# Kernel tuning notes

Hardware: AMD Instinct MI355X
Metric: run time of the kernel (lower is better)

## Reference

```python
import jax, jax.numpy as jnp
import numpy as np

N, E = 100000, 1600000
NODE_DIM, EDGE_DIM, HIDDEN = 64, 32, 64


def setup_inputs() -> dict:
    key = jax.random.key(0)
    ks = jax.random.split(key, 12)
    def lin(k, fan_in, fan_out):
        bound = 1.0 / np.sqrt(fan_in)
        kw, kb = jax.random.split(k)
        W = jax.random.uniform(kw, (fan_in, fan_out), jnp.float32, -bound, bound)
        b = jax.random.uniform(kb, (fan_out,), jnp.float32, -bound, bound)
        return W, b
    h = jax.random.normal(ks[0], (N, NODE_DIM), jnp.float32)
    edge_index = jax.random.randint(ks[1], (2, E), 0, N, jnp.int64 if jax.config.jax_enable_x64 else jnp.int32)
    edge_feat = jax.random.normal(ks[2], (E, EDGE_DIM), jnp.float32)
    eW1, eb1 = lin(ks[3], 2 * NODE_DIM + EDGE_DIM, HIDDEN)
    eW2, eb2 = lin(ks[4], HIDDEN, HIDDEN)
    uW1, ub1 = lin(ks[5], NODE_DIM + HIDDEN, HIDDEN)
    uW2, ub2 = lin(ks[6], HIDDEN, HIDDEN)
    return {"h": h, "edge_index": edge_index, "edge_feat": edge_feat,
            "eW1": eW1, "eb1": eb1, "eW2": eW2, "eb2": eb2,
            "uW1": uW1, "ub1": ub1, "uW2": uW2, "ub2": ub2}


def reference(h, edge_index, edge_feat, eW1, eb1, eW2, eb2, uW1, ub1, uW2, ub2):
    src, tgt = edge_index[0], edge_index[1]
    # gather endpoint features, concat with edge features: (E, 2*node_dim+edge_dim)
    inp = jnp.concatenate([h[src], h[tgt], edge_feat], axis=-1)
    # edge MLP: Linear -> ReLU -> Linear
    messages = jax.nn.relu(inp @ eW1 + eb1) @ eW2 + eb2  # (E, hidden)
    # scatter-add aggregation onto target nodes
    agg = jax.ops.segment_sum(messages, tgt, num_segments=h.shape[0])  # (N, hidden)
    # update MLP on [h || agg]
    upd_in = jnp.concatenate([h, agg], axis=-1)
    out = jax.nn.relu(upd_in @ uW1 + ub1) @ uW2 + ub2  # (N, hidden)
    return out
```

## Files before the change

### kernel.cpp

```cpp
#include <hip/hip_runtime.h>
#include <hip/hip_bf16.h>


typedef __attribute__((ext_vector_type(8))) short s16x8;
typedef __attribute__((ext_vector_type(4))) float f32x4;
typedef __attribute__((ext_vector_type(8))) unsigned short u16x8;

#define SXE 168
#define SXN 136
#define SX2 72
#define NBLK_EDGE 768
#define S1_CHUNK 4096
#define S2_CAP 10240

__device__ __forceinline__ unsigned short f2bf(float f) {
  __hip_bfloat16 b = __float2bfloat16(f);
  return __builtin_bit_cast(unsigned short, b);
}
__device__ __forceinline__ float bf2f(unsigned short s) {
  unsigned int u = ((unsigned int)s) << 16;
  return __builtin_bit_cast(float, u);
}
__device__ __forceinline__ u16x8 pack8(const float4 a, const float4 b) {
  u16x8 r;
  r[0] = f2bf(a.x); r[1] = f2bf(a.y); r[2] = f2bf(a.z); r[3] = f2bf(a.w);
  r[4] = f2bf(b.x); r[5] = f2bf(b.y); r[6] = f2bf(b.z); r[7] = f2bf(b.w);
  return r;
}

__device__ __forceinline__ void bar_lgkm() {
  __builtin_amdgcn_sched_barrier(0);
  asm volatile("s_waitcnt lgkmcnt(0)" ::: "memory");
  __builtin_amdgcn_s_barrier();
  __builtin_amdgcn_sched_barrier(0);
}

__global__ void prep(const float* __restrict__ h, unsigned short* __restrict__ hb, long long htot,
                     const float* __restrict__ eW1, const float* __restrict__ eW2,
                     const float* __restrict__ uW1, const float* __restrict__ uW2,
                     unsigned short* __restrict__ w1p, unsigned short* __restrict__ w2p,
                     unsigned short* __restrict__ uw1p, unsigned short* __restrict__ uw2p,
                     const int* __restrict__ ei, int* __restrict__ bhist, int E,
                     int conv_blocks) {
  __shared__ int lh[256];
  const int b = blockIdx.x;
  const int tid = threadIdx.x;
  if (b < conv_blocks) {
    const long long i = ((long long)b * 256 + tid) * 4;
    if (i + 3 < htot) {
      const float4 v = *(const float4*)(h + i);
      ushort4 o;
      o.x = f2bf(v.x); o.y = f2bf(v.y); o.z = f2bf(v.z); o.w = f2bf(v.w);
      *(ushort4*)(hb + i) = o;
    } else {
      for (long long j = i; j < htot; ++j) hb[j] = f2bf(h[j]);
    }
  } else if (b < conv_blocks + 13) {
    const int t2 = (b - conv_blocks) * 256 + tid;
    if (t2 < 52 * 64) {
      const int c = t2 & 63;
      int kg = t2 >> 6;
      const float* src;
      unsigned short* dst;
      if (kg < 20)      { src = eW1; dst = w1p; }
      else if (kg < 28) { src = eW2; dst = w2p; kg -= 20; }
      else if (kg < 44) { src = uW1; dst = uw1p; kg -= 28; }
      else              { src = uW2; dst = uw2p; kg -= 44; }
#pragma unroll
      for (int e = 0; e < 8; ++e)
        dst[(size_t)(kg * 64 + c) * 8 + e] = f2bf(src[(size_t)(kg * 8 + e) * 64 + c]);
    }
  } else {
    lh[tid] = 0;
    __syncthreads();
    const int hbk = b - conv_blocks - 13;
    for (long long e = (long long)hbk * 256 + tid; e < E; e += 1024LL * 256)
      atomicAdd(&lh[ei[E + e] >> 9], 1);
    __syncthreads();
    if (lh[tid]) atomicAdd(&bhist[tid], lh[tid]);
  }
}

__global__ void bscan(const int* __restrict__ bhist, int* __restrict__ bstart,
                      int* __restrict__ bcursor, int nbuck) {
  __shared__ int s[256];
  const int tid = threadIdx.x;
  const int v = (tid < nbuck) ? bhist[tid] : 0;
  s[tid] = v;
  __syncthreads();
  for (int off = 1; off < 256; off <<= 1) {
    int t = (tid >= off) ? s[tid - off] : 0;
    __syncthreads();
    s[tid] += t;
    __syncthreads();
  }
  const int excl = s[tid] - v;
  if (tid < nbuck) { bstart[tid] = excl; bcursor[tid] = excl; }
}

__global__ __launch_bounds__(256)
void bucket_scatter(const int* __restrict__ ei, int* __restrict__ bcursor,
                    unsigned long long* __restrict__ bufA, int E) {
  __shared__ int lhist[256], lbase[256], lcur[256];
  const int tid = threadIdx.x;
  const long long c0 = (long long)blockIdx.x * S1_CHUNK;

  lhist[tid] = 0;
  __syncthreads();

  unsigned long long rec[16];
  int bk[16];
#pragma unroll
  for (int j = 0; j < 16; ++j) {
    const long long e = c0 + j * 256 + tid;
    if (e < E) {
      const int t = ei[E + e];
      const int s = ei[e];
      rec[j] = (unsigned long long)(unsigned int)e |
               ((unsigned long long)(unsigned int)t << 21) |
               ((unsigned long long)(unsigned int)s << 38);
      bk[j] = t >> 9;
      atomicAdd(&lhist[bk[j]], 1);
    } else {
      bk[j] = -1;
    }
  }
  __syncthreads();

  if (lhist[tid] > 0) lbase[tid] = atomicAdd(&bcursor[tid], lhist[tid]);
  lcur[tid] = 0;
  __syncthreads();

#pragma unroll
  for (int j = 0; j < 16; ++j) {
    if (bk[j] >= 0) {
      const int pos = lbase[bk[j]] + atomicAdd(&lcur[bk[j]], 1);
      bufA[pos] = rec[j];
    }
  }
}

__global__ __launch_bounds__(256)
void bucket_sort(const unsigned long long* __restrict__ bufA,
                 const int* __restrict__ bstart, const int* __restrict__ bhist,
                 unsigned long long* __restrict__ aoe) {
  __shared__ unsigned long long srec[S2_CAP];
  __shared__ int khist[512];
  __shared__ int sdata[256];
  const int b = blockIdx.x;
  const int tid = threadIdx.x;
  const int s0 = bstart[b];
  const int nb = bhist[b];

  if (nb > S2_CAP) {
    for (int i = tid; i < nb; i += 256) aoe[s0 + i] = bufA[s0 + i];
    return;
  }

  khist[tid] = 0;
  khist[tid + 256] = 0;
  __syncthreads();
  for (int i = tid; i < nb; i += 256) {
    const unsigned long long r = bufA[s0 + i];
    atomicAdd(&khist[(int)((r >> 21) & 511)], 1);
  }
  __syncthreads();

  const int a0 = khist[2 * tid], a1 = khist[2 * tid + 1];
  const int sum = a0 + a1;
  sdata[tid] = sum;
  __syncthreads();
  for (int off = 1; off < 256; off <<= 1) {
    int t = (tid >= off) ? sdata[tid - off] : 0;
    __syncthreads();
    sdata[tid] += t;
    __syncthreads();
  }
  const int excl = sdata[tid] - sum;
  khist[2 * tid] = excl;
  khist[2 * tid + 1] = excl + a0;
  __syncthreads();

  for (int i = tid; i < nb; i += 256) {
    const unsigned long long r = bufA[s0 + i];
    const int pos = atomicAdd(&khist[(int)((r >> 21) & 511)], 1);
    srec[pos] = r;
  }
  __syncthreads();
  for (int i = tid; i < nb; i += 256) aoe[s0 + i] = srec[i];
}

__global__ __launch_bounds__(256, 4)
void edge_mlp_fused(const unsigned short* __restrict__ hb, const float* __restrict__ ef,
                    const unsigned short* __restrict__ w1p, const float* __restrict__ b1,
                    const unsigned short* __restrict__ w2p, const float* __restrict__ b2,
                    const unsigned long long* __restrict__ aoe, float* __restrict__ agg,
                    int E, int ntiles, int nblk) {
  __shared__ unsigned short X[64 * SXE];
  __shared__ unsigned short X2[64 * SX2];
  __shared__ unsigned short W2L[64 * 64];
  __shared__ int tgts[2][64];

  const int tid = threadIdx.x;
  const int w = tid >> 6, lane = tid & 63;
  const int g = lane >> 4, r = lane & 15;
  const int row = tid >> 2, q = tid & 3;

  {
    const int i = tid * 16;
    *(u16x8*)&W2L[i] = *(const u16x8*)&w2p[i];
    *(u16x8*)&W2L[i + 8] = *(const u16x8*)&w2p[i + 8];
  }

  const int t0 = (int)((long long)blockIdx.x * ntiles / nblk);
  const int t1 = (int)((long long)(blockIdx.x + 1) * ntiles / nblk);
  if (t0 >= t1) return;

  const long long Emax = (long long)E - 1;
  const int cb = w * 16;

  s16x8 bfrag1[5];
#pragma unroll
  for (int kk = 0; kk < 5; ++kk)
    bfrag1[kk] = *(const s16x8*)(w1p + (size_t)((kk * 4 + g) * 64 + cb + r) * 8);
  const float bias1 = b1[cb + r];
  float b2v[4];
#pragma unroll
  for (int nb = 0; nb < 4; ++nb) b2v[nb] = b2[nb * 16 + r];

  unsigned long long nxt_aoe;
  u16x8 hs0, hs1, ht0, ht1;
  float4 fea, feb;

  auto load_aoe = [&](int t) -> unsigned long long {
    long long p = (long long)t * 64 + row;
    if (p > Emax) p = Emax;
    return aoe[p];
  };
  auto issue_gathers = [&](const unsigned long long u) {
    const int s = (int)(u >> 38);
    const int t = (int)((u >> 21) & 0x1FFFF);
    const int e = (int)(u & 0x1FFFFF);
    const u16x8* hs = (const u16x8*)(hb + (size_t)s * 64);
    const u16x8* ht = (const u16x8*)(hb + (size_t)t * 64);
    hs0 = hs[2 * q]; hs1 = hs[2 * q + 1];
    ht0 = ht[2 * q]; ht1 = ht[2 * q + 1];
    const float4* fp = (const float4*)(ef + (size_t)e * 32);
    fea = fp[2 * q]; feb = fp[2 * q + 1];
  };
  auto write_tile = [&](int t, const unsigned long long u) {
    *(u16x8*)&X[row * SXE + 16 * q] = hs0;
    *(u16x8*)&X[row * SXE + 16 * q + 8] = hs1;
    *(u16x8*)&X[row * SXE + 64 + 16 * q] = ht0;
    *(u16x8*)&X[row * SXE + 64 + 16 * q + 8] = ht1;
    *(u16x8*)&X[row * SXE + 128 + 8 * q] = pack8(fea, feb);
    if (q == 0) tgts[t & 1][row] = ((long long)t * 64 + row < E)
                                       ? (int)((u >> 21) & 0x1FFFF) : -1;
  };

  {
    const unsigned long long a0 = load_aoe(t0);
    nxt_aoe = load_aoe(t0 + 1 < t1 ? t0 + 1 : t0);
    issue_gathers(a0);
    write_tile(t0, a0);
  }
  bar_lgkm();

  for (int t = t0; t < t1; ++t) {
    const bool have_next = (t + 1 < t1);

    unsigned long long ga = nxt_aoe;
    if (have_next) {
      nxt_aoe = load_aoe(t + 2 < t1 ? t + 2 : t + 1);
      issue_gathers(ga);
    }

    f32x4 acc[4];
    acc[0] = acc[1] = acc[2] = acc[3] = (f32x4){bias1, bias1, bias1, bias1};
    __builtin_amdgcn_s_setprio(1);
#pragma unroll
    for (int kk = 0; kk < 5; ++kk) {
#pragma unroll
      for (int er = 0; er < 4; ++er) {
        const s16x8 af = *(const s16x8*)&X[(er * 16 + r) * SXE + kk * 32 + 8 * g];
        acc[er] = __builtin_amdgcn_mfma_f32_16x16x32_bf16(af, bfrag1[kk], acc[er], 0, 0, 0);
      }
    }
    __builtin_amdgcn_s_setprio(0);

    bar_lgkm();

#pragma unroll
    for (int er = 0; er < 4; ++er)
#pragma unroll
      for (int i = 0; i < 4; ++i)
        X2[(er * 16 + 4 * g + i) * SX2 + cb + r] = f2bf(fmaxf(acc[er][i], 0.0f));
    if (have_next) write_tile(t + 1, ga);

    bar_lgkm();

    const s16x8 af0 = *(const s16x8*)&X2[(16 * w + r) * SX2 + 8 * g];
    const s16x8 af1 = *(const s16x8*)&X2[(16 * w + r) * SX2 + 32 + 8 * g];
    f32x4 acc2[4];
#pragma unroll
    for (int nb = 0; nb < 4; ++nb)
      acc2[nb] = (f32x4){b2v[nb], b2v[nb], b2v[nb], b2v[nb]};
    __builtin_amdgcn_s_setprio(1);
#pragma unroll
    for (int nb = 0; nb < 4; ++nb) {
      const s16x8 bf0 = *(const s16x8*)&W2L[(size_t)((0 + g) * 64 + nb * 16 + r) * 8];
      const s16x8 bf1 = *(const s16x8*)&W2L[(size_t)((4 + g) * 64 + nb * 16 + r) * 8];
      acc2[nb] = __builtin_amdgcn_mfma_f32_16x16x32_bf16(af0, bf0, acc2[nb], 0, 0, 0);
      acc2[nb] = __builtin_amdgcn_mfma_f32_16x16x32_bf16(af1, bf1, acc2[nb], 0, 0, 0);
    }
    __builtin_amdgcn_s_setprio(0);

#pragma unroll
    for (int nb = 0; nb < 4; ++nb)
#pragma unroll
      for (int i = 0; i < 4; ++i)
        X2[(16 * w + 4 * g + i) * SX2 + nb * 16 + r] = f2bf(acc2[nb][i]);
    asm volatile("s_waitcnt lgkmcnt(0)" ::: "memory");
    __builtin_amdgcn_sched_barrier(0);

    {
      float sum = 0.0f;
      int curt = -1;
#pragma unroll 4
      for (int i = 0; i < 16; ++i) {
        const int rr = 16 * w + i;
        const int tt = tgts[t & 1][rr];
        const float v = bf2f(X2[rr * SX2 + lane]);
        if (tt != curt) {
          if (curt >= 0) atomicAdd(agg + (size_t)curt * 64 + lane, sum);
          curt = tt;
          sum = 0.0f;
        }
        if (tt >= 0) sum += v;
      }
      if (curt >= 0) atomicAdd(agg + (size_t)curt * 64 + lane, sum);
    }
  }
}

__global__ __launch_bounds__(256, 4)
void node_mlp_mfma(const unsigned short* __restrict__ hb, const float* __restrict__ agg,
                   const unsigned short* __restrict__ w1p, const float* __restrict__ b1,
                   const unsigned short* __restrict__ w2p, const float* __restrict__ b2,
                   float* __restrict__ out, int N) {
  __shared__ unsigned short X[64 * SXN];
  __shared__ unsigned short X2[64 * SX2];

  const int tid = threadIdx.x;
  const int w = tid >> 6, lane = tid & 63;
  const int g = lane >> 4, r = lane & 15;
  const long long base = (long long)blockIdx.x * 64;

  {
    const int row = tid >> 2, q = tid & 3;
    long long n = base + row;
    if (n >= N) n = N - 1;
    const u16x8* hr = (const u16x8*)(hb + (size_t)n * 64);
    *(u16x8*)&X[row * SXN + 16 * q] = hr[2 * q];
    *(u16x8*)&X[row * SXN + 16 * q + 8] = hr[2 * q + 1];
    const float4* ar = (const float4*)(agg + (size_t)n * 64);
    *(u16x8*)&X[row * SXN + 64 + 16 * q] = pack8(ar[4 * q], ar[4 * q + 1]);
    *(u16x8*)&X[row * SXN + 64 + 16 * q + 8] = pack8(ar[4 * q + 2], ar[4 * q + 3]);
  }
  __syncthreads();

  const int cb = w * 16;

  const float bias1 = b1[cb + r];
  f32x4 acc[4];
  acc[0] = acc[1] = acc[2] = acc[3] = (f32x4){bias1, bias1, bias1, bias1};
#pragma unroll
  for (int kk = 0; kk < 4; ++kk) {
    const s16x8 bf = *(const s16x8*)(w1p + (size_t)((kk * 4 + g) * 64 + cb + r) * 8);
#pragma unroll
    for (int er = 0; er < 4; ++er) {
      const s16x8 af = *(const s16x8*)&X[(er * 16 + r) * SXN + kk * 32 + 8 * g];
      acc[er] = __builtin_amdgcn_mfma_f32_16x16x32_bf16(af, bf, acc[er], 0, 0, 0);
    }
  }

#pragma unroll
  for (int er = 0; er < 4; ++er)
#pragma unroll
    for (int i = 0; i < 4; ++i)
      X2[(er * 16 + 4 * g + i) * SX2 + cb + r] = f2bf(fmaxf(acc[er][i], 0.0f));
  __syncthreads();

  const float bias2 = b2[cb + r];
  f32x4 a2[4];
  a2[0] = a2[1] = a2[2] = a2[3] = (f32x4){bias2, bias2, bias2, bias2};
#pragma unroll
  for (int kk = 0; kk < 2; ++kk) {
    const s16x8 bf = *(const s16x8*)(w2p + (size_t)((kk * 4 + g) * 64 + cb + r) * 8);
#pragma unroll
    for (int er = 0; er < 4; ++er) {
      const s16x8 af = *(const s16x8*)&X2[(er * 16 + r) * SX2 + kk * 32 + 8 * g];
      a2[er] = __builtin_amdgcn_mfma_f32_16x16x32_bf16(af, bf, a2[er], 0, 0, 0);
    }
  }

#pragma unroll
  for (int er = 0; er < 4; ++er)
#pragma unroll
    for (int i = 0; i < 4; ++i) {
      const long long n = base + er * 16 + 4 * g + i;
      if (n < N) out[n * 64 + cb + r] = a2[er][i];
    }
}

extern "C" void kernel_launch(void* const* d_in, const int* in_sizes, int n_in,
                              void* d_out, int out_size, void* d_ws, size_t ws_size,
                              hipStream_t stream) {
  const float* h   = (const float*)d_in[0];
  const int*   ei  = (const int*)d_in[1];
  const float* ef  = (const float*)d_in[2];
  const float* eW1 = (const float*)d_in[3];
  const float* eb1 = (const float*)d_in[4];
  const float* eW2 = (const float*)d_in[5];
  const float* eb2 = (const float*)d_in[6];
  const float* uW1 = (const float*)d_in[7];
  const float* ub1 = (const float*)d_in[8];
  const float* uW2 = (const float*)d_in[9];
  const float* ub2 = (const float*)d_in[10];
  float* out = (float*)d_out;

  const int N = in_sizes[0] / 64;
  const int E = in_sizes[1] / 2;
  const int NBUCK = (N + 511) >> 9;
  const int ntiles = (E + 63) / 64;
  const int nblk = ntiles < NBLK_EDGE ? ntiles : NBLK_EDGE;

  size_t off = 0;
  auto alloc = [&](size_t bytes) { size_t o = off; off += (bytes + 255) & ~(size_t)255; return o; };
  const size_t agg_off    = alloc((size_t)N * 64 * 4);
  const size_t bhist_off  = alloc(256 * 4);
  const size_t bstart_off = alloc(256 * 4);
  const size_t bcur_off   = alloc(256 * 4);
  const size_t hb_off     = alloc((size_t)N * 64 * 2);
  const size_t w1p_off    = alloc((size_t)160 * 64 * 2);
  const size_t w2p_off    = alloc((size_t)64 * 64 * 2);
  const size_t uw1p_off   = alloc((size_t)128 * 64 * 2);
  const size_t uw2p_off   = alloc((size_t)64 * 64 * 2);
  const size_t bufA_off   = alloc((size_t)E * 8);
  const size_t aoe_off    = alloc((size_t)E * 8);
  char* ws = (char*)d_ws;

  float*          agg  = (float*)(ws + agg_off);
  int*            bhist = (int*)(ws + bhist_off);
  int*            bstart = (int*)(ws + bstart_off);
  int*            bcursor = (int*)(ws + bcur_off);
  unsigned short* hb   = (unsigned short*)(ws + hb_off);
  unsigned short* w1p  = (unsigned short*)(ws + w1p_off);
  unsigned short* w2p  = (unsigned short*)(ws + w2p_off);
  unsigned short* uw1p = (unsigned short*)(ws + uw1p_off);
  unsigned short* uw2p = (unsigned short*)(ws + uw2p_off);
  unsigned long long* bufA = (unsigned long long*)(ws + bufA_off);
  unsigned long long* aoe  = (unsigned long long*)(ws + aoe_off);

  hipMemsetAsync(ws + agg_off, 0, bhist_off + 256 * 4 - agg_off, stream);

  const long long htot = (long long)N * 64;
  const int conv_blocks = (int)((htot / 4 + 255) / 256);
  prep<<<conv_blocks + 13 + 1024, 256, 0, stream>>>(h, hb, htot, eW1, eW2, uW1, uW2,
                                                    w1p, w2p, uw1p, uw2p, ei, bhist, E,
                                                    conv_blocks);

  bscan<<<1, 256, 0, stream>>>(bhist, bstart, bcursor, NBUCK);
  bucket_scatter<<<(E + S1_CHUNK - 1) / S1_CHUNK, 256, 0, stream>>>(ei, bcursor, bufA, E);
  bucket_sort<<<NBUCK, 256, 0, stream>>>(bufA, bstart, bhist, aoe);

  edge_mlp_fused<<<nblk, 256, 0, stream>>>(hb, ef, w1p, eb1, w2p, eb2, aoe, agg, E, ntiles, nblk);
  node_mlp_mfma<<<(N + 63) / 64, 256, 0, stream>>>(hb, agg, uw1p, ub1, uw2p, ub2, out, N);
}
```

Measured before the change: 222.7 us.

## Make edge MLP tiles wave-local and drop block barriers in the loop

The first edge GEMM is repartitioned so each wave computes all 64 hidden columns for its own 16 edge rows. It reads W1 fragments from a new LDS copy instead of holding per-wave column slices in registers. Because each wave now produces, consumes and scatters only rows it gathered itself, the block-wide barriers inside the tile loop become LDS waits. W2 fragments are read straight from global memory, relying on cache, and the occupancy hint drops from 4 to 3 blocks to fit the larger LDS footprint. This is meant to cut barrier stalls between waves, at the cost of extra LDS use, lower occupancy and repeated global reads of W2.

```diff
diff --git a/kernel.cpp b/kernel.cpp
--- a/kernel.cpp
+++ b/kernel.cpp
@@ -27,11 +27,9 @@
   r[4] = f2bf(b.x); r[5] = f2bf(b.y); r[6] = f2bf(b.z); r[7] = f2bf(b.w);
   return r;
 }
-
-__device__ __forceinline__ void bar_lgkm() {
+__device__ __forceinline__ void wait_lds() {
   __builtin_amdgcn_sched_barrier(0);
   asm volatile("s_waitcnt lgkmcnt(0)" ::: "memory");
-  __builtin_amdgcn_s_barrier();
   __builtin_amdgcn_sched_barrier(0);
 }
 
@@ -190,7 +188,7 @@
   for (int i = tid; i < nb; i += 256) aoe[s0 + i] = srec[i];
 }
 
-__global__ __launch_bounds__(256, 4)
+__global__ __launch_bounds__(256, 3)
 void edge_mlp_fused(const unsigned short* __restrict__ hb, const float* __restrict__ ef,
                     const unsigned short* __restrict__ w1p, const float* __restrict__ b1,
                     const unsigned short* __restrict__ w2p, const float* __restrict__ b2,
@@ -198,7 +196,7 @@
                     int E, int ntiles, int nblk) {
   __shared__ unsigned short X[64 * SXE];
   __shared__ unsigned short X2[64 * SX2];
-  __shared__ unsigned short W2L[64 * 64];
+  __shared__ unsigned short W1L[160 * 64];
   __shared__ int tgts[2][64];
 
   const int tid = threadIdx.x;
@@ -206,27 +204,18 @@
   const int g = lane >> 4, r = lane & 15;
   const int row = tid >> 2, q = tid & 3;
 
-  {
-    const int i = tid * 16;
-    *(u16x8*)&W2L[i] = *(const u16x8*)&w2p[i];
-    *(u16x8*)&W2L[i + 8] = *(const u16x8*)&w2p[i + 8];
-  }
+  for (int i = tid; i < 1280; i += 256)
+    *(u16x8*)&W1L[(size_t)i * 8] = *(const u16x8*)&w1p[(size_t)i * 8];
 
   const int t0 = (int)((long long)blockIdx.x * ntiles / nblk);
   const int t1 = (int)((long long)(blockIdx.x + 1) * ntiles / nblk);
-  if (t0 >= t1) return;
+  if (t0 >= t1) { __syncthreads(); return; }
 
   const long long Emax = (long long)E - 1;
-  const int cb = w * 16;
-
-  s16x8 bfrag1[5];
-#pragma unroll
-  for (int kk = 0; kk < 5; ++kk)
-    bfrag1[kk] = *(const s16x8*)(w1p + (size_t)((kk * 4 + g) * 64 + cb + r) * 8);
-  const float bias1 = b1[cb + r];
-  float b2v[4];
-#pragma unroll
-  for (int nb = 0; nb < 4; ++nb) b2v[nb] = b2[nb * 16 + r];
+
+  float b1v[4], b2v[4];
+#pragma unroll
+  for (int nb = 0; nb < 4; ++nb) { b1v[nb] = b1[nb * 16 + r]; b2v[nb] = b2[nb * 16 + r]; }
 
   unsigned long long nxt_aoe;
   u16x8 hs0, hs1, ht0, ht1;
@@ -264,7 +253,7 @@
     issue_gathers(a0);
     write_tile(t0, a0);
   }
-  bar_lgkm();
+  __syncthreads();
 
   for (int t = t0; t < t1; ++t) {
     const bool have_next = (t + 1 < t1);
@@ -276,28 +265,28 @@
     }
 
     f32x4 acc[4];
-    acc[0] = acc[1] = acc[2] = acc[3] = (f32x4){bias1, bias1, bias1, bias1};
+#pragma unroll
+    for (int nb = 0; nb < 4; ++nb)
+      acc[nb] = (f32x4){b1v[nb], b1v[nb], b1v[nb], b1v[nb]};
     __builtin_amdgcn_s_setprio(1);
 #pragma unroll
     for (int kk = 0; kk < 5; ++kk) {
-#pragma unroll
-      for (int er = 0; er < 4; ++er) {
-        const s16x8 af = *(const s16x8*)&X[(er * 16 + r) * SXE + kk * 32 + 8 * g];
-        acc[er] = __builtin_amdgcn_mfma_f32_16x16x32_bf16(af, bfrag1[kk], acc[er], 0, 0, 0);
+      const s16x8 af = *(const s16x8*)&X[(16 * w + r) * SXE + kk * 32 + 8 * g];
+#pragma unroll
+      for (int nb = 0; nb < 4; ++nb) {
+        const s16x8 bf = *(const s16x8*)&W1L[(size_t)((kk * 4 + g) * 64 + nb * 16 + r) * 8];
+        acc[nb] = __builtin_amdgcn_mfma_f32_16x16x32_bf16(af, bf, acc[nb], 0, 0, 0);
       }
     }
     __builtin_amdgcn_s_setprio(0);
 
-    bar_lgkm();
-
-#pragma unroll
-    for (int er = 0; er < 4; ++er)
+#pragma unroll
+    for (int nb = 0; nb < 4; ++nb)
 #pragma unroll
       for (int i = 0; i < 4; ++i)
-        X2[(er * 16 + 4 * g + i) * SX2 + cb + r] = f2bf(fmaxf(acc[er][i], 0.0f));
+        X2[(16 * w + 4 * g + i) * SX2 + nb * 16 + r] = f2bf(fmaxf(acc[nb][i], 0.0f));
     if (have_next) write_tile(t + 1, ga);
-
-    bar_lgkm();
+    wait_lds();
 
     const s16x8 af0 = *(const s16x8*)&X2[(16 * w + r) * SX2 + 8 * g];
     const s16x8 af1 = *(const s16x8*)&X2[(16 * w + r) * SX2 + 32 + 8 * g];
@@ -308,8 +297,8 @@
     __builtin_amdgcn_s_setprio(1);
 #pragma unroll
     for (int nb = 0; nb < 4; ++nb) {
-      const s16x8 bf0 = *(const s16x8*)&W2L[(size_t)((0 + g) * 64 + nb * 16 + r) * 8];
-      const s16x8 bf1 = *(const s16x8*)&W2L[(size_t)((4 + g) * 64 + nb * 16 + r) * 8];
+      const s16x8 bf0 = *(const s16x8*)(w2p + (size_t)((0 + g) * 64 + nb * 16 + r) * 8);
+      const s16x8 bf1 = *(const s16x8*)(w2p + (size_t)((4 + g) * 64 + nb * 16 + r) * 8);
       acc2[nb] = __builtin_amdgcn_mfma_f32_16x16x32_bf16(af0, bf0, acc2[nb], 0, 0, 0);
       acc2[nb] = __builtin_amdgcn_mfma_f32_16x16x32_bf16(af1, bf1, acc2[nb], 0, 0, 0);
     }
@@ -320,8 +309,7 @@
 #pragma unroll
       for (int i = 0; i < 4; ++i)
         X2[(16 * w + 4 * g + i) * SX2 + nb * 16 + r] = f2bf(acc2[nb][i]);
-    asm volatile("s_waitcnt lgkmcnt(0)" ::: "memory");
-    __builtin_amdgcn_sched_barrier(0);
+    wait_lds();
 
     {
       float sum = 0.0f;
@@ -340,6 +328,7 @@
       }
       if (curt >= 0) atomicAdd(agg + (size_t)curt * 64 + lane, sum);
     }
+    wait_lds();
   }
 }
 
```

New measurement: 223.2 us. About the same (+0.2%).
